# Kernel optimization log

Hardware: AMD Instinct MI355X
Metric: run time of the kernel (lower is better)

## Reference

```python
import jax, jax.numpy as jnp
import numpy as np

BS, SEQ_LEN, DIM = 8, 16, 512
DIM_QK, DIM_V = 512, 512
MAX_BS, MAX_SEQ = 8, 8192
START_POS = 4096
KV_LEN = START_POS + SEQ_LEN


def setup_inputs() -> dict:
    key = jax.random.key(0)
    ks = jax.random.split(key, 8)
    w_scale = 0.02
    return {
        "x": jax.random.normal(ks[0], (BS, SEQ_LEN, DIM), dtype=jnp.float32),
        "start_pos": START_POS,
        "mask": jnp.zeros((SEQ_LEN, KV_LEN), dtype=jnp.float32),
        "Wq": jax.random.normal(ks[1], (DIM_QK, DIM), dtype=jnp.float32) * w_scale,
        "Wk": jax.random.normal(ks[2], (DIM_QK, DIM), dtype=jnp.float32) * w_scale,
        "Wv": jax.random.normal(ks[3], (DIM_V, DIM), dtype=jnp.float32) * w_scale,
        "Wo": jax.random.normal(ks[4], (DIM, DIM_V), dtype=jnp.float32) * w_scale,
        "cache_k": jax.random.normal(ks[5], (MAX_BS, MAX_SEQ, DIM_QK), dtype=jnp.float32) * 0.1,
        "cache_v": jax.random.normal(ks[6], (MAX_BS, MAX_SEQ, DIM_V), dtype=jnp.float32) * 0.1,
    }


def reference(x, start_pos, mask, Wq, Wk, Wv, Wo, cache_k, cache_v):
    bs, seq_len, _ = x.shape
    dim_qk = Wq.shape[0]
    scale = (dim_qk // 2) ** (-0.5)  # note: source uses dim_qk//2, not dim_qk

    # projections (torch Linear: y = x @ W.T, W is [out, in])
    q = jnp.einsum('bsd,ed->bse', x, Wq)
    k = jnp.einsum('bsd,ed->bse', x, Wk)
    v = jnp.einsum('bsd,ed->bse', x, Wv)

    # KV-cache append + read (start_pos is static)
    cache_k = jax.lax.dynamic_update_slice(cache_k, k, (0, start_pos, 0))
    cache_v = jax.lax.dynamic_update_slice(cache_v, v, (0, start_pos, 0))
    k_full = cache_k[:bs, :start_pos + seq_len]  # [bs, kv_len, dim_qk]
    v_full = cache_v[:bs, :start_pos + seq_len]  # [bs, kv_len, dim_v]

    dist = jnp.einsum('bqd,bkd->bqk', q, k_full) * scale  # [bs, q, kv]
    weight = jax.lax.stop_gradient(dist)
    dist = dist + mask  # additive mask, broadcast over batch
    probs = jax.nn.softmax(dist, axis=-1)
    atten = jnp.einsum('bqk,bkv->bqv', probs, v_full)
    out = jnp.einsum('bqv,ev->bqe', atten, Wo)
    return (out, weight)
```

## Files before the change

kernel.cpp:

```cpp
#include <hip/hip_runtime.h>

#define BSZ 8
#define SEQ 16
#define DIMN 512
#define SP 4096
#define KVL 4112

#define SCALE 0.0625f

#define PPART 0
#define QBUF  786432
#define KNEW  851968
#define VNEW  917504
#define PROBS 983040
#define APART 1509376
#define ATTEN 5769216
#define OPART 5834752

__global__ __launch_bounds__(64) void proj_partial(
    const float* __restrict__ X, const float* __restrict__ W0,
    const float* __restrict__ W1, const float* __restrict__ W2,
    float* __restrict__ outbase)
{
  __shared__ float xs[SEQ][128];
  int b = blockIdx.x >> 2, et = blockIdx.x & 3;
  int dt = blockIdx.y, m = blockIdx.z;
  const float* W = (m == 0) ? W0 : (m == 1) ? W1 : W2;
  float* outp = outbase + (size_t)m * (4 * 65536) + (size_t)dt * 65536;
  int t = threadIdx.x;

  const float4* xsrc = (const float4*)(X + (size_t)(b * SEQ) * DIMN + dt * 128);
  for (int i = t; i < SEQ * 32; i += 64) {
    int row = i >> 5, j = i & 31;
    *(float4*)&xs[row][j * 4] = xsrc[row * 128 + j];
  }
  __syncthreads();

  int r0 = (t >> 5) * 8;
  int e = et * 128 + (t & 31) * 4;
  float acc[8][4];
#pragma unroll
  for (int r = 0; r < 8; ++r)
#pragma unroll
    for (int i = 0; i < 4; ++i) acc[r][i] = 0.f;

  const float* wbase = W + dt * 128;
  for (int d4 = 0; d4 < 32; ++d4) {
    float4 w[4];
#pragma unroll
    for (int i = 0; i < 4; ++i)
      w[i] = *(const float4*)(wbase + (size_t)(e + i) * DIMN + d4 * 4);
#pragma unroll
    for (int r = 0; r < 8; ++r) {
      float4 xv = *(const float4*)&xs[r0 + r][d4 * 4];
#pragma unroll
      for (int i = 0; i < 4; ++i)
        acc[r][i] += xv.x * w[i].x + xv.y * w[i].y + xv.z * w[i].z + xv.w * w[i].w;
    }
  }
#pragma unroll
  for (int r = 0; r < 8; ++r) {
    float4 o = make_float4(acc[r][0], acc[r][1], acc[r][2], acc[r][3]);
    *(float4*)(outp + (size_t)(b * SEQ + r0 + r) * DIMN + e) = o;
  }
}

__global__ __launch_bounds__(256) void reduce_dt(
    const float* __restrict__ src, float* __restrict__ dst, int nm)
{
  int idx = blockIdx.x * 256 + threadIdx.x;
  if (idx >= nm * 65536) return;
  int m = idx >> 16, j = idx & 65535;
  const float* s = src + (size_t)m * (4 * 65536);
  dst[idx] = s[j] + s[65536 + j] + s[2 * 65536 + j] + s[3 * 65536 + j];
}

__global__ __launch_bounds__(256) void scores_kernel(
    const float* __restrict__ qbuf, const float* __restrict__ cache_k,
    const float* __restrict__ knew, float* __restrict__ weight)
{
  int b = blockIdx.x;
  int p0 = blockIdx.y * 64;
  int len = KVL - p0; if (len > 64) len = 64;
  int t = threadIdx.x, lane = t & 63, w = t >> 6;

  float4 qa[SEQ], qb[SEQ];
  const float* qbase = qbuf + (size_t)b * SEQ * DIMN + lane * 8;
#pragma unroll
  for (int s = 0; s < SEQ; ++s) {
    qa[s] = *(const float4*)(qbase + s * DIMN);
    qb[s] = *(const float4*)(qbase + s * DIMN + 4);
  }

  bool b1 = (lane & 1), b2 = (lane & 2), b4 = (lane & 4), b8 = (lane & 8);
  int niter = (len - w + 3) >> 2;
#pragma unroll 2
  for (int i = 0; i < niter; ++i) {
    int p = p0 + w + 4 * i;
    const float* krow = (p < SP)
        ? (cache_k + ((size_t)b * 8192 + p) * DIMN)
        : (knew + (size_t)(b * SEQ + (p - SP)) * DIMN);
    float4 ka = *(const float4*)(krow + lane * 8);
    float4 kb = *(const float4*)(krow + lane * 8 + 4);

    float acc[SEQ];
#pragma unroll
    for (int s = 0; s < SEQ; ++s) {
      acc[s] = qa[s].x * ka.x + qa[s].y * ka.y + qa[s].z * ka.z + qa[s].w * ka.w
             + qb[s].x * kb.x + qb[s].y * kb.y + qb[s].z * kb.z + qb[s].w * kb.w;
    }
    float r8[8];
#pragma unroll
    for (int u = 0; u < 8; ++u) {
      float keep = b1 ? acc[u + 8] : acc[u];
      float send = b1 ? acc[u] : acc[u + 8];
      r8[u] = keep + __shfl_xor(send, 1);
    }
    float r4[4];
#pragma unroll
    for (int u = 0; u < 4; ++u) {
      float keep = b2 ? r8[u + 4] : r8[u];
      float send = b2 ? r8[u] : r8[u + 4];
      r4[u] = keep + __shfl_xor(send, 2);
    }
    float r2[2];
#pragma unroll
    for (int u = 0; u < 2; ++u) {
      float keep = b4 ? r4[u + 2] : r4[u];
      float send = b4 ? r4[u] : r4[u + 2];
      r2[u] = keep + __shfl_xor(send, 4);
    }
    float keep = b8 ? r2[1] : r2[0];
    float send = b8 ? r2[0] : r2[1];
    float r1 = keep + __shfl_xor(send, 8);
    r1 += __shfl_xor(r1, 16);
    r1 += __shfl_xor(r1, 32);

    if (lane < 16) {
      int s = ((lane & 1) << 3) | ((lane & 2) << 1) | ((lane & 4) >> 1) | ((lane & 8) >> 3);
      weight[(size_t)(b * SEQ + s) * KVL + p] = r1 * SCALE;
    }
  }
}

__global__ __launch_bounds__(256) void softmax_kernel(
    const float* __restrict__ weight, const float* __restrict__ mask,
    float* __restrict__ probs)
{
  int row = blockIdx.x;
  int s = row & 15;
  int t = threadIdx.x, lane = t & 63, w = t >> 6;
  const float* src = weight + (size_t)row * KVL;
  const float* msk = mask + (size_t)s * KVL;

  float vals[17];
  float mx = -1e30f;
#pragma unroll
  for (int i = 0; i < 17; ++i) {
    int p = t + i * 256;
    if (p < KVL) { vals[i] = src[p] + msk[p]; mx = fmaxf(mx, vals[i]); }
    else vals[i] = -1e30f;
  }
  for (int off = 32; off >= 1; off >>= 1) mx = fmaxf(mx, __shfl_xor(mx, off));
  __shared__ float redm[4], reds[4];
  if (lane == 0) redm[w] = mx;
  __syncthreads();
  mx = fmaxf(fmaxf(redm[0], redm[1]), fmaxf(redm[2], redm[3]));

  float sum = 0.f;
#pragma unroll
  for (int i = 0; i < 17; ++i) {
    int p = t + i * 256;
    if (p < KVL) { vals[i] = __expf(vals[i] - mx); sum += vals[i]; }
  }
  for (int off = 32; off >= 1; off >>= 1) sum += __shfl_xor(sum, off);
  if (lane == 0) reds[w] = sum;
  __syncthreads();
  sum = reds[0] + reds[1] + reds[2] + reds[3];
  float inv = 1.0f / sum;

  float* dst = probs + (size_t)row * KVL;
#pragma unroll
  for (int i = 0; i < 17; ++i) {
    int p = t + i * 256;
    if (p < KVL) dst[p] = vals[i] * inv;
  }
}

__global__ __launch_bounds__(256) void attnv_kernel(
    const float* __restrict__ probs, const float* __restrict__ cache_v,
    const float* __restrict__ vnew, float* __restrict__ apart)
{
  __shared__ float pl[SEQ][64];
  int b = blockIdx.x, c = blockIdx.y;
  int p0 = c * 64;
  int len = KVL - p0; if (len > 64) len = 64;
  int t = threadIdx.x;

  for (int i = t; i < SEQ * 64; i += 256) {
    int q = i >> 6, j = i & 63;
    pl[q][j] = (j < len) ? probs[(size_t)(b * SEQ + q) * KVL + p0 + j] : 0.f;
  }
  __syncthreads();

  float acc0[SEQ], acc1[SEQ];
#pragma unroll
  for (int q = 0; q < SEQ; ++q) { acc0[q] = 0.f; acc1[q] = 0.f; }

  int nj4 = len >> 2;
  for (int j4 = 0; j4 < nj4; ++j4) {
    float4 pv[SEQ];
#pragma unroll
    for (int q = 0; q < SEQ; ++q) pv[q] = *(const float4*)&pl[q][j4 * 4];
#pragma unroll
    for (int jj = 0; jj < 4; ++jj) {
      int p = p0 + j4 * 4 + jj;
      const float* vrow = (p < SP)
          ? (cache_v + ((size_t)b * 8192 + p) * DIMN)
          : (vnew + (size_t)(b * SEQ + (p - SP)) * DIMN);
      float va = vrow[t], vb = vrow[t + 256];
#pragma unroll
      for (int q = 0; q < SEQ; ++q) {
        float pj = (jj == 0) ? pv[q].x : (jj == 1) ? pv[q].y : (jj == 2) ? pv[q].z : pv[q].w;
        acc0[q] += pj * va;
        acc1[q] += pj * vb;
      }
    }
  }
  float* outp = apart + (size_t)c * 65536 + (size_t)b * SEQ * DIMN;
#pragma unroll
  for (int q = 0; q < SEQ; ++q) {
    outp[q * DIMN + t] = acc0[q];
    outp[q * DIMN + t + 256] = acc1[q];
  }
}

__global__ __launch_bounds__(256) void reduce_att(
    const float* __restrict__ apart, float* __restrict__ atten)
{
  int idx = blockIdx.x * 256 + threadIdx.x;
  float s = 0.f;
  for (int c = 0; c < 65; ++c) s += apart[(size_t)c * 65536 + idx];
  atten[idx] = s;
}

extern "C" void kernel_launch(void* const* d_in, const int* in_sizes, int n_in,
                              void* d_out, int out_size, void* d_ws, size_t ws_size,
                              hipStream_t stream) {
  const float* x       = (const float*)d_in[0];
  const float* mask    = (const float*)d_in[2];
  const float* Wq      = (const float*)d_in[3];
  const float* Wk      = (const float*)d_in[4];
  const float* Wv      = (const float*)d_in[5];
  const float* Wo      = (const float*)d_in[6];
  const float* cache_k = (const float*)d_in[7];
  const float* cache_v = (const float*)d_in[8];
  float* out    = (float*)d_out;
  float* weight = out + 65536;
  float* ws     = (float*)d_ws;

  proj_partial<<<dim3(32, 4, 3), 64, 0, stream>>>(x, Wq, Wk, Wv, ws + PPART);
  reduce_dt<<<dim3(768), 256, 0, stream>>>(ws + PPART, ws + QBUF, 3);
  scores_kernel<<<dim3(8, 65), 256, 0, stream>>>(ws + QBUF, cache_k, ws + KNEW, weight);
  softmax_kernel<<<dim3(128), 256, 0, stream>>>(weight, mask, ws + PROBS);
  attnv_kernel<<<dim3(8, 65), 256, 0, stream>>>(ws + PROBS, cache_v, ws + VNEW, ws + APART);
  reduce_att<<<dim3(256), 256, 0, stream>>>(ws + APART, ws + ATTEN);
  proj_partial<<<dim3(32, 4, 1), 64, 0, stream>>>(ws + ATTEN, Wo, Wo, Wo, ws + OPART);
  reduce_dt<<<dim3(256), 256, 0, stream>>>(ws + OPART, out, 1);
}
```

Before: 324.3 us.

## Drop split-K projection reductions and split scores query rows across wave pairs

Projections now compute the full 512-wide dot product in one 256-thread block, writing Q/K/V and the output directly instead of writing per-slice partials and summing them in separate reduce kernels. This removes two launches and the partial-sum traffic, at the cost of fewer, longer-running blocks (96 and 32 blocks). The scores kernel now has each wave handle 8 query rows instead of 16, with two waves per row group striding positions by 2. This halves the per-thread q registers and shortens the shuffle tree, but each K row is now loaded by two waves instead of one.

Measured after the change: 410.7 us. +26.6%, slower.

```diff
diff --git a/kernel.cpp b/kernel.cpp
--- a/kernel.cpp
+++ b/kernel.cpp
@@ -8,50 +8,46 @@
 
 #define SCALE 0.0625f
 
-#define PPART 0
-#define QBUF  786432
-#define KNEW  851968
-#define VNEW  917504
-#define PROBS 983040
-#define APART 1509376
-#define ATTEN 5769216
-#define OPART 5834752
-
-__global__ __launch_bounds__(64) void proj_partial(
+#define QBUF  0
+#define KNEW  65536
+#define VNEW  131072
+#define PROBS 196608
+#define APART 722944
+#define ATTEN 4982784
+
+__global__ __launch_bounds__(256) void proj_full(
     const float* __restrict__ X, const float* __restrict__ W0,
     const float* __restrict__ W1, const float* __restrict__ W2,
-    float* __restrict__ outbase)
-{
-  __shared__ float xs[SEQ][128];
+    float* __restrict__ O0, float* __restrict__ O1, float* __restrict__ O2)
+{
+  __shared__ float xs[SEQ][DIMN];
   int b = blockIdx.x >> 2, et = blockIdx.x & 3;
-  int dt = blockIdx.y, m = blockIdx.z;
+  int m = blockIdx.y;
   const float* W = (m == 0) ? W0 : (m == 1) ? W1 : W2;
-  float* outp = outbase + (size_t)m * (4 * 65536) + (size_t)dt * 65536;
+  float* O = (m == 0) ? O0 : (m == 1) ? O1 : O2;
   int t = threadIdx.x;
 
-  const float4* xsrc = (const float4*)(X + (size_t)(b * SEQ) * DIMN + dt * 128);
-  for (int i = t; i < SEQ * 32; i += 64) {
-    int row = i >> 5, j = i & 31;
-    *(float4*)&xs[row][j * 4] = xsrc[row * 128 + j];
-  }
-  __syncthreads();
-
-  int r0 = (t >> 5) * 8;
+  const float4* xsrc = (const float4*)(X + (size_t)b * SEQ * DIMN);
+  float4* xdst = (float4*)&xs[0][0];
+#pragma unroll
+  for (int i = 0; i < 8; ++i) xdst[t + i * 256] = xsrc[t + i * 256];
+  __syncthreads();
+
   int e = et * 128 + (t & 31) * 4;
-  float acc[8][4];
-#pragma unroll
-  for (int r = 0; r < 8; ++r)
+  int r0 = (t >> 5) * 2;
+  float acc[2][4];
+#pragma unroll
+  for (int r = 0; r < 2; ++r)
 #pragma unroll
     for (int i = 0; i < 4; ++i) acc[r][i] = 0.f;
 
-  const float* wbase = W + dt * 128;
-  for (int d4 = 0; d4 < 32; ++d4) {
+  for (int d4 = 0; d4 < 128; ++d4) {
     float4 w[4];
 #pragma unroll
     for (int i = 0; i < 4; ++i)
-      w[i] = *(const float4*)(wbase + (size_t)(e + i) * DIMN + d4 * 4);
-#pragma unroll
-    for (int r = 0; r < 8; ++r) {
+      w[i] = *(const float4*)(W + (size_t)(e + i) * DIMN + d4 * 4);
+#pragma unroll
+    for (int r = 0; r < 2; ++r) {
       float4 xv = *(const float4*)&xs[r0 + r][d4 * 4];
 #pragma unroll
       for (int i = 0; i < 4; ++i)
@@ -59,20 +55,10 @@
     }
   }
 #pragma unroll
-  for (int r = 0; r < 8; ++r) {
+  for (int r = 0; r < 2; ++r) {
     float4 o = make_float4(acc[r][0], acc[r][1], acc[r][2], acc[r][3]);
-    *(float4*)(outp + (size_t)(b * SEQ + r0 + r) * DIMN + e) = o;
-  }
-}
-
-__global__ __launch_bounds__(256) void reduce_dt(
-    const float* __restrict__ src, float* __restrict__ dst, int nm)
-{
-  int idx = blockIdx.x * 256 + threadIdx.x;
-  if (idx >= nm * 65536) return;
-  int m = idx >> 16, j = idx & 65535;
-  const float* s = src + (size_t)m * (4 * 65536);
-  dst[idx] = s[j] + s[65536 + j] + s[2 * 65536 + j] + s[3 * 65536 + j];
+    *(float4*)(O + (size_t)(b * SEQ + r0 + r) * DIMN + e) = o;
+  }
 }
 
 __global__ __launch_bounds__(256) void scores_kernel(
@@ -83,62 +69,56 @@
   int p0 = blockIdx.y * 64;
   int len = KVL - p0; if (len > 64) len = 64;
   int t = threadIdx.x, lane = t & 63, w = t >> 6;
-
-  float4 qa[SEQ], qb[SEQ];
-  const float* qbase = qbuf + (size_t)b * SEQ * DIMN + lane * 8;
-#pragma unroll
-  for (int s = 0; s < SEQ; ++s) {
+  int qg = w >> 1, par = w & 1;
+
+  float4 qa[8], qb[8];
+  const float* qbase = qbuf + ((size_t)b * SEQ + qg * 8) * DIMN + lane * 8;
+#pragma unroll
+  for (int s = 0; s < 8; ++s) {
     qa[s] = *(const float4*)(qbase + s * DIMN);
     qb[s] = *(const float4*)(qbase + s * DIMN + 4);
   }
 
-  bool b1 = (lane & 1), b2 = (lane & 2), b4 = (lane & 4), b8 = (lane & 8);
-  int niter = (len - w + 3) >> 2;
-#pragma unroll 2
+  bool b1 = (lane & 1), b2 = (lane & 2), b4 = (lane & 4);
+  int niter = (len - par + 1) >> 1;
   for (int i = 0; i < niter; ++i) {
-    int p = p0 + w + 4 * i;
+    int p = p0 + par + 2 * i;
     const float* krow = (p < SP)
         ? (cache_k + ((size_t)b * 8192 + p) * DIMN)
         : (knew + (size_t)(b * SEQ + (p - SP)) * DIMN);
     float4 ka = *(const float4*)(krow + lane * 8);
     float4 kb = *(const float4*)(krow + lane * 8 + 4);
 
-    float acc[SEQ];
-#pragma unroll
-    for (int s = 0; s < SEQ; ++s) {
+    float acc[8];
+#pragma unroll
+    for (int s = 0; s < 8; ++s) {
       acc[s] = qa[s].x * ka.x + qa[s].y * ka.y + qa[s].z * ka.z + qa[s].w * ka.w
              + qb[s].x * kb.x + qb[s].y * kb.y + qb[s].z * kb.z + qb[s].w * kb.w;
     }
-    float r8[8];
-#pragma unroll
-    for (int u = 0; u < 8; ++u) {
-      float keep = b1 ? acc[u + 8] : acc[u];
-      float send = b1 ? acc[u] : acc[u + 8];
-      r8[u] = keep + __shfl_xor(send, 1);
-    }
     float r4[4];
 #pragma unroll
     for (int u = 0; u < 4; ++u) {
-      float keep = b2 ? r8[u + 4] : r8[u];
-      float send = b2 ? r8[u] : r8[u + 4];
-      r4[u] = keep + __shfl_xor(send, 2);
+      float keep = b1 ? acc[u + 4] : acc[u];
+      float send = b1 ? acc[u] : acc[u + 4];
+      r4[u] = keep + __shfl_xor(send, 1);
     }
     float r2[2];
 #pragma unroll
     for (int u = 0; u < 2; ++u) {
-      float keep = b4 ? r4[u + 2] : r4[u];
-      float send = b4 ? r4[u] : r4[u + 2];
-      r2[u] = keep + __shfl_xor(send, 4);
-    }
-    float keep = b8 ? r2[1] : r2[0];
-    float send = b8 ? r2[0] : r2[1];
-    float r1 = keep + __shfl_xor(send, 8);
+      float keep = b2 ? r4[u + 2] : r4[u];
+      float send = b2 ? r4[u] : r4[u + 2];
+      r2[u] = keep + __shfl_xor(send, 2);
+    }
+    float keep = b4 ? r2[1] : r2[0];
+    float send = b4 ? r2[0] : r2[1];
+    float r1 = keep + __shfl_xor(send, 4);
+    r1 += __shfl_xor(r1, 8);
     r1 += __shfl_xor(r1, 16);
     r1 += __shfl_xor(r1, 32);
 
-    if (lane < 16) {
-      int s = ((lane & 1) << 3) | ((lane & 2) << 1) | ((lane & 4) >> 1) | ((lane & 8) >> 3);
-      weight[(size_t)(b * SEQ + s) * KVL + p] = r1 * SCALE;
+    if (lane < 8) {
+      int s = ((lane & 1) << 2) | (lane & 2) | ((lane & 4) >> 2);
+      weight[(size_t)(b * SEQ + qg * 8 + s) * KVL + p] = r1 * SCALE;
     }
   }
 }
@@ -259,12 +239,12 @@
   float* weight = out + 65536;
   float* ws     = (float*)d_ws;
 
-  proj_partial<<<dim3(32, 4, 3), 64, 0, stream>>>(x, Wq, Wk, Wv, ws + PPART);
-  reduce_dt<<<dim3(768), 256, 0, stream>>>(ws + PPART, ws + QBUF, 3);
+  proj_full<<<dim3(32, 3), 256, 0, stream>>>(
+      x, Wq, Wk, Wv, ws + QBUF, ws + KNEW, ws + VNEW);
   scores_kernel<<<dim3(8, 65), 256, 0, stream>>>(ws + QBUF, cache_k, ws + KNEW, weight);
   softmax_kernel<<<dim3(128), 256, 0, stream>>>(weight, mask, ws + PROBS);
   attnv_kernel<<<dim3(8, 65), 256, 0, stream>>>(ws + PROBS, cache_v, ws + VNEW, ws + APART);
   reduce_att<<<dim3(256), 256, 0, stream>>>(ws + APART, ws + ATTEN);
-  proj_partial<<<dim3(32, 4, 1), 64, 0, stream>>>(ws + ATTEN, Wo, Wo, Wo, ws + OPART);
-  reduce_dt<<<dim3(256), 256, 0, stream>>>(ws + OPART, out, 1);
-}
+  proj_full<<<dim3(32, 1), 256, 0, stream>>>(
+      ws + ATTEN, Wo, Wo, Wo, out, out, out);
+}
```
